# Performance work log

Hardware: AMD Instinct MI355X
Metric: run time of the kernel (lower is better)

The kernel has to match this reference:

```python
import jax, jax.numpy as jnp
import numpy as np

N = 4096   # num ROIs across the batch (sgdet: ~8 images x 512 proposals)
H = 256    # rl_input_size == rl_hidden_size (hard-coded in __init__)
C = 151    # Visual Genome object classes incl. background


def setup_inputs() -> dict:
    key = jax.random.key(0)
    ks = jax.random.split(key, 7)
    prepro_feat = jax.random.normal(ks[0], (N, H), jnp.float32)
    d = jax.random.uniform(ks[1], (N, C), jnp.float32)
    obj_distributions = d / d.sum(-1, keepdims=True)  # softmax-like class probs
    co_occour = jax.random.uniform(ks[2], (C, C), jnp.float32)
    W_sub = jax.random.normal(ks[3], (H, H), jnp.float32) / np.sqrt(H)
    b_sub = jnp.zeros((H,), jnp.float32)
    W_obj = jax.random.normal(ks[4], (H, H), jnp.float32) / np.sqrt(H)
    b_obj = jnp.zeros((H,), jnp.float32)
    w_scores = jax.random.normal(ks[5], (3 * H + 3,), jnp.float32) / np.sqrt(3 * H + 3)
    b_scores = jnp.zeros((), jnp.float32)
    return dict(prepro_feat=prepro_feat, obj_distributions=obj_distributions,
                co_occour=co_occour, W_sub=W_sub, b_sub=b_sub,
                W_obj=W_obj, b_obj=b_obj, w_scores=w_scores, b_scores=b_scores)


def reference(prepro_feat, obj_distributions, co_occour, W_sub, b_sub,
              W_obj, b_obj, w_scores, b_scores):
    n = prepro_feat.shape[0]
    h = W_sub.shape[1]
    # label_scores = co_occour.sum(1)
    label_scores = co_occour.sum(1)                                   # [C]
    # rl_sub/rl_obj Linear + ReLU. In the torch expand, pair (i,j) uses sub[j], obj[i].
    sub = jax.nn.relu(prepro_feat @ W_sub + b_sub)                    # [N,H]
    obj = jax.nn.relu(prepro_feat @ W_obj + b_obj)                    # [N,H]
    # pair_score[i,j] = sum_{a,b} dist[j,a] * dist[i,b] * co[a,b]  (detached)
    pair_score = jax.lax.stop_gradient(
        jnp.einsum('ja,ab,ib->ij', obj_distributions, co_occour, obj_distributions))  # [N,N]
    s = jax.lax.stop_gradient(obj_distributions @ label_scores)       # [N]
    sub_score = s[None, :]   # varies along j
    obj_score = s[:, None]   # varies along i
    # rl_scores Linear over concat(sub*obj, sub, obj, pair, sub_score, obj_score),
    # decomposed exactly into its blocks (avoids the [N,N,3H+3] intermediate).
    w_mul, w_s, w_o = w_scores[:h], w_scores[h:2 * h], w_scores[2 * h:3 * h]
    w_ps, w_ss, w_os = w_scores[3 * h], w_scores[3 * h + 1], w_scores[3 * h + 2]
    pair_out = ((obj * w_mul) @ sub.T                                 # [i,j] = sum_h obj[i,h]*sub[j,h]*w_mul[h]
                + (sub @ w_s)[None, :]
                + (obj @ w_o)[:, None]
                + w_ps * pair_score + w_ss * sub_score + w_os * obj_score
                + b_scores)                                           # [N,N]
    pair_gates = jax.nn.sigmoid(pair_out).reshape(-1, 1)              # [N*N, 1]
    return pair_gates
```

## Files before the change

kernel.cpp:

```cpp
#include <hip/hip_runtime.h>
#include <hip/hip_bf16.h>
#include <math.h>

#define N_DIM 4096
#define H_DIM 256
#define C_DIM 151
#define KP    448
#define KT    160

typedef unsigned short ushort_t;
typedef __attribute__((ext_vector_type(8))) short bf16x8;
typedef __attribute__((ext_vector_type(4))) float f32x4;

#define WSB_PPACK  0
#define WSB_WT     2097152
#define WSB_DPACK  2359296
#define WSB_COT    3670016
#define WSB_PART   3731456
#define WSB_SPART  3993600
#define WSB_APACK  4091904
#define WSB_BPACK  7761920

#define GLL(src, dst) __builtin_amdgcn_global_load_lds( \
    (const __attribute__((address_space(1))) void*)(src), \
    (__attribute__((address_space(3))) void*)(dst), 16, 0, 0)

__global__ __launch_bounds__(256) void k_cvt(
    const float* __restrict__ P, const float* __restrict__ Ws,
    const float* __restrict__ Wo, const float* __restrict__ D,
    const float* __restrict__ co, const float* __restrict__ wsc,
    __hip_bfloat16* __restrict__ Pp, __hip_bfloat16* __restrict__ Wt,
    __hip_bfloat16* __restrict__ Dpack, __hip_bfloat16* __restrict__ coT,
    __hip_bfloat16* __restrict__ Apack) {
    __shared__ float shbuf[64 * C_DIM];
    const int t = threadIdx.x;
    const int bid = blockIdx.x;
    if (bid < 512) {
        int idx = (bid * 256 + t) * 8;
        float4 a = *(const float4*)(P + idx);
        float4 b = *(const float4*)(P + idx + 4);
        __hip_bfloat16 h[8];
        h[0] = __float2bfloat16(a.x); h[1] = __float2bfloat16(a.y);
        h[2] = __float2bfloat16(a.z); h[3] = __float2bfloat16(a.w);
        h[4] = __float2bfloat16(b.x); h[5] = __float2bfloat16(b.y);
        h[6] = __float2bfloat16(b.z); h[7] = __float2bfloat16(b.w);
        *(bf16x8*)&Pp[idx] = *(bf16x8*)h;
    } else if (bid < 544) {
        const int b  = bid - 512;
        const int k0 = (b & 3) * 64;
        const int h0 = ((b >> 2) & 3) * 64;
        const int z  = b >> 4;
        const float* W = z ? Wo : Ws;
        #pragma unroll
        for (int q = 0; q < 4; ++q) {
            int r = (t >> 4) + q * 16;
            int c = (t & 15) * 4;
            float4 f = *(const float4*)&W[(size_t)(k0 + r) * H_DIM + h0 + c];
            shbuf[r * 65 + c] = f.x; shbuf[r * 65 + c + 1] = f.y;
            shbuf[r * 65 + c + 2] = f.z; shbuf[r * 65 + c + 3] = f.w;
        }
        __syncthreads();
        #pragma unroll
        for (int q = 0; q < 2; ++q) {
            int idx = t + q * 256;
            int h   = idx >> 3;
            int kc  = idx & 7;
            __hip_bfloat16 u[8];
            #pragma unroll
            for (int j = 0; j < 8; ++j)
                u[j] = __float2bfloat16(shbuf[(kc * 8 + j) * 65 + h]);
            *(bf16x8*)&Wt[((size_t)z * H_DIM + h0 + h) * H_DIM + k0 + kc * 8] = *(bf16x8*)u;
        }
    } else if (bid < 608) {
        const int b  = bid - 544;
        const int i0 = b * 64;
        for (int idx = t; idx < 64 * C_DIM; idx += 256)
            shbuf[idx] = D[(size_t)i0 * C_DIM + idx];
        __syncthreads();
        const float wps = wsc[768];
        for (int o = t; o < 64 * (KT / 8); o += 256) {
            int r = o / (KT / 8), ch = o % (KT / 8);
            __hip_bfloat16 u[8];
            #pragma unroll
            for (int j = 0; j < 8; ++j) {
                int k = ch * 8 + j;
                u[j] = __float2bfloat16(k < C_DIM ? shbuf[r * C_DIM + k] : 0.f);
            }
            *(bf16x8*)&Dpack[(size_t)(i0 + r) * KT + ch * 8] = *(bf16x8*)u;
        }
        for (int o = t; o < 64 * 24; o += 256) {
            int r = o / 24, ch = o % 24;
            __hip_bfloat16 u[8];
            #pragma unroll
            for (int j = 0; j < 8; ++j) {
                int c = ch * 8 + j;
                u[j] = __float2bfloat16(c < C_DIM ? wps * shbuf[r * C_DIM + c] : 0.f);
            }
            *(bf16x8*)&Apack[(size_t)(i0 + r) * KP + H_DIM + ch * 8] = *(bf16x8*)u;
        }
    } else {
        const int q  = bid - 608;
        const int a0 = (q % 3) * 64;
        const int c0 = (q / 3) * 64;
        for (int o = t; o < 64 * 64; o += 256) {
            int r = o >> 6, c = o & 63;
            float v = 0.f;
            if (a0 + r < C_DIM && c0 + c < C_DIM)
                v = co[(size_t)(a0 + r) * C_DIM + c0 + c];
            shbuf[r * 65 + c] = v;
        }
        __syncthreads();
        const int nch = (a0 == 128) ? 4 : 8;
        for (int o = t; o < 64 * 8; o += 256) {
            int cl = o >> 3, ch = o & 7;
            if (ch < nch) {
                __hip_bfloat16 u[8];
                #pragma unroll
                for (int j = 0; j < 8; ++j)
                    u[j] = __float2bfloat16(shbuf[(ch * 8 + j) * 65 + cl]);
                *(bf16x8*)&coT[(size_t)(c0 + cl) * KT + a0 + ch * 8] = *(bf16x8*)u;
            }
        }
    }
}

__global__ __launch_bounds__(256) void k_mid(
    const ushort_t* __restrict__ Pp, const ushort_t* __restrict__ Wt,
    const ushort_t* __restrict__ Dpack, const ushort_t* __restrict__ coT,
    const float* __restrict__ bsub, const float* __restrict__ bobj,
    const float* __restrict__ wsc,
    __hip_bfloat16* __restrict__ Apack, __hip_bfloat16* __restrict__ Bpack,
    float* __restrict__ part, float* __restrict__ spart) {
    __shared__ ushort_t As[128 * 256];
    __shared__ ushort_t Bs[64 * 256];

    const int t = threadIdx.x;
    const int w = t >> 6, l = t & 63;
    const int wr = w >> 1, wc = w & 1;
    const int lr = l & 15, g = l >> 4;
    const int bid = blockIdx.x;

    if (bid < 256) {
        const int hblk = bid & 3;
        const int i0   = ((bid >> 2) & 31) * 128;
        const int z    = bid >> 7;
        const int j0   = hblk * 64;
        const float* bias = z ? bobj : bsub;
        const ushort_t* Wz = Wt + (size_t)z * H_DIM * H_DIM;

        #pragma unroll
        for (int r_ = 0; r_ < 16; ++r_) {
            int idx = t + r_ * 256, row = idx >> 5, cl = idx & 31;
            int cs = cl ^ (row & 7);
            GLL(Pp + (size_t)(i0 + row) * H_DIM + cs * 8, &As[idx * 8]);
        }
        #pragma unroll
        for (int r_ = 0; r_ < 8; ++r_) {
            int idx = t + r_ * 256, row = idx >> 5, cl = idx & 31;
            int cs = cl ^ (row & 7);
            GLL(Wz + (size_t)(j0 + row) * H_DIM + cs * 8, &Bs[idx * 8]);
        }
        __syncthreads();

        f32x4 acc[4][2];
        #pragma unroll
        for (int m = 0; m < 4; ++m)
            #pragma unroll
            for (int n = 0; n < 2; ++n) acc[m][n] = f32x4{0.f, 0.f, 0.f, 0.f};

        #pragma unroll
        for (int ks2 = 0; ks2 < 8; ++ks2) {
            bf16x8 a[4], b[2];
            int c = ks2 * 4 + g;
            #pragma unroll
            for (int m = 0; m < 4; ++m) {
                int Rl = wr * 64 + m * 16 + lr;
                int cl = c ^ (Rl & 7);
                a[m] = *(const bf16x8*)&As[(Rl * 32 + cl) * 8];
            }
            #pragma unroll
            for (int n = 0; n < 2; ++n) {
                int Rl = wc * 32 + n * 16 + lr;
                int cl = c ^ (Rl & 7);
                b[n] = *(const bf16x8*)&Bs[(Rl * 32 + cl) * 8];
            }
            #pragma unroll
            for (int m = 0; m < 4; ++m)
                #pragma unroll
                for (int n = 0; n < 2; ++n)
                    acc[m][n] = __builtin_amdgcn_mfma_f32_16x16x32_bf16(
                        a[m], b[n], acc[m][n], 0, 0, 0);
        }

        int hn[2]; float bb[2], wse[2], wmu[2];
        #pragma unroll
        for (int n = 0; n < 2; ++n) {
            hn[n]  = j0 + wc * 32 + n * 16 + lr;
            bb[n]  = bias[hn[n]];
            wse[n] = wsc[(z ? 512 : 256) + hn[n]];
            wmu[n] = wsc[hn[n]];
        }
        float* partq = part + (size_t)(z * 8 + hblk * 2 + wc) * N_DIM;
        #pragma unroll
        for (int m = 0; m < 4; ++m) {
            float p[4] = {0.f, 0.f, 0.f, 0.f};
            #pragma unroll
            for (int n = 0; n < 2; ++n)
                #pragma unroll
                for (int r = 0; r < 4; ++r) {
                    float v = acc[m][n][r] + bb[n];
                    v = v > 0.f ? v : 0.f;
                    int i = i0 + wr * 64 + m * 16 + g * 4 + r;
                    if (z) Apack[(size_t)i * KP + hn[n]] = __float2bfloat16(v * wmu[n]);
                    else   Bpack[(size_t)i * KP + hn[n]] = __float2bfloat16(v);
                    p[r] += v * wse[n];
                }
            #pragma unroll
            for (int r = 0; r < 4; ++r) {
                p[r] += __shfl_xor(p[r], 1);
                p[r] += __shfl_xor(p[r], 2);
                p[r] += __shfl_xor(p[r], 4);
                p[r] += __shfl_xor(p[r], 8);
            }
            if (lr == 0)
                #pragma unroll
                for (int r = 0; r < 4; ++r)
                    partq[i0 + wr * 64 + m * 16 + g * 4 + r] = p[r];
        }
    } else {
        const int q  = bid - 256;
        const int j0 = (q % 3) * 64;
        const int i0 = (q / 3) * 64;

        bf16x8 a[2][5], b[2][5];
        #pragma unroll
        for (int m = 0; m < 2; ++m) {
            const ushort_t* ap = Dpack + (size_t)(i0 + wr * 32 + m * 16 + lr) * KT + g * 8;
            #pragma unroll
            for (int ks = 0; ks < 5; ++ks) a[m][ks] = *(const bf16x8*)(ap + ks * 32);
        }
        #pragma unroll
        for (int n = 0; n < 2; ++n) {
            const ushort_t* bp = coT + (size_t)(j0 + wc * 32 + n * 16 + lr) * KT + g * 8;
            #pragma unroll
            for (int ks = 0; ks < 5; ++ks) b[n][ks] = *(const bf16x8*)(bp + ks * 32);
        }

        f32x4 acc[2][2];
        #pragma unroll
        for (int m = 0; m < 2; ++m)
            #pragma unroll
            for (int n = 0; n < 2; ++n) acc[m][n] = f32x4{0.f, 0.f, 0.f, 0.f};
        #pragma unroll
        for (int ks = 0; ks < 5; ++ks)
            #pragma unroll
            for (int m = 0; m < 2; ++m)
                #pragma unroll
                for (int n = 0; n < 2; ++n)
                    acc[m][n] = __builtin_amdgcn_mfma_f32_16x16x32_bf16(
                        a[m][ks], b[n][ks], acc[m][n], 0, 0, 0);

        float* sp = spart + (size_t)((q % 3) * 2 + wc) * N_DIM;
        #pragma unroll
        for (int m = 0; m < 2; ++m) {
            float p[4] = {0.f, 0.f, 0.f, 0.f};
            #pragma unroll
            for (int n = 0; n < 2; ++n) {
                int col = j0 + wc * 32 + n * 16 + lr;
                #pragma unroll
                for (int r = 0; r < 4; ++r) {
                    int i = i0 + wr * 32 + m * 16 + g * 4 + r;
                    float v = acc[m][n][r];
                    Bpack[(size_t)i * KP + H_DIM + col] = __float2bfloat16(v);
                    p[r] += v;
                }
            }
            #pragma unroll
            for (int r = 0; r < 4; ++r) {
                p[r] += __shfl_xor(p[r], 1);
                p[r] += __shfl_xor(p[r], 2);
                p[r] += __shfl_xor(p[r], 4);
                p[r] += __shfl_xor(p[r], 8);
            }
            if (lr == 0)
                #pragma unroll
                for (int r = 0; r < 4; ++r)
                    sp[i0 + wr * 32 + m * 16 + g * 4 + r] = p[r];
        }
    }
}

__global__ __launch_bounds__(512) void k_main(
    const ushort_t* __restrict__ Apack, const ushort_t* __restrict__ Bpack,
    const float* __restrict__ part, const float* __restrict__ spart,
    const float* __restrict__ wsc, const float* __restrict__ bsc,
    float* __restrict__ out) {
    __shared__ ushort_t pool[(256 + 128) * 64];
    __shared__ float rbS[256], cbS[128];
    ushort_t* As = pool;
    ushort_t* Bs = pool + 256 * 64;

    const int t = threadIdx.x;
    const int w = t >> 6, l = t & 63;
    const int wm = w >> 1, wn = w & 1;
    const int lr = l & 15, g = l >> 4;
    const int bid = blockIdx.x;
    const int swz = (bid & 7) * 64 + (bid >> 3);
    const int i0 = (swz >> 5) * 256;
    const int j0 = (swz & 31) * 128;

#define K_STAGE(ks) do {                                                        \
    _Pragma("unroll")                                                           \
    for (int r_ = 0; r_ < 4; ++r_) {                                            \
        int idx_ = t + r_ * 512, row_ = idx_ >> 3, cl_ = idx_ & 7;              \
        int cs_ = cl_ ^ (row_ & 7);                                             \
        GLL(Apack + (size_t)(i0+row_)*KP + (ks)*64 + cs_*8, &As[idx_*8]);       \
    }                                                                           \
    _Pragma("unroll")                                                           \
    for (int r_ = 0; r_ < 2; ++r_) {                                            \
        int idx_ = t + r_ * 512, row_ = idx_ >> 3, cl_ = idx_ & 7;              \
        int cs_ = cl_ ^ (row_ & 7);                                             \
        GLL(Bpack + (size_t)(j0+row_)*KP + (ks)*64 + cs_*8, &Bs[idx_*8]);       \
    }                                                                           \
} while (0)

#define K_COMPUTE() do {                                                        \
    _Pragma("unroll")                                                           \
    for (int ks2 = 0; ks2 < 2; ++ks2) {                                         \
        bf16x8 a[4], b[4];                                                      \
        int c = ks2 * 4 + g;                                                    \
        _Pragma("unroll")                                                       \
        for (int m_ = 0; m_ < 4; ++m_) {                                        \
            int Rl = wm * 64 + m_ * 16 + lr;                                    \
            int cl = c ^ (Rl & 7);                                              \
            a[m_] = *(const bf16x8*)&As[(Rl * 8 + cl) * 8];                     \
        }                                                                       \
        _Pragma("unroll")                                                       \
        for (int n_ = 0; n_ < 4; ++n_) {                                        \
            int Rl = wn * 64 + n_ * 16 + lr;                                    \
            int cl = c ^ (Rl & 7);                                              \
            b[n_] = *(const bf16x8*)&Bs[(Rl * 8 + cl) * 8];                     \
        }                                                                       \
        _Pragma("unroll")                                                       \
        for (int m_ = 0; m_ < 4; ++m_)                                          \
            _Pragma("unroll")                                                   \
            for (int n_ = 0; n_ < 4; ++n_)                                      \
                acc[m_][n_] = __builtin_amdgcn_mfma_f32_16x16x32_bf16(          \
                    a[m_], b[n_], acc[m_][n_], 0, 0, 0);                        \
    }                                                                           \
} while (0)

    K_STAGE(0);
    if (t < 256) {
        int i = i0 + t; float r = 0.f, si = 0.f;
        #pragma unroll
        for (int q = 8; q < 16; ++q) r += part[(size_t)q * N_DIM + i];
        #pragma unroll
        for (int q = 0; q < 6; ++q) si += spart[(size_t)q * N_DIM + i];
        rbS[t] = r + wsc[770] * si;
    } else if (t < 384) {
        int j = j0 + (t - 256); float c = 0.f, sj = 0.f;
        #pragma unroll
        for (int q = 0; q < 8; ++q) c += part[(size_t)q * N_DIM + j];
        #pragma unroll
        for (int q = 0; q < 6; ++q) sj += spart[(size_t)q * N_DIM + j];
        cbS[t - 256] = c + wsc[769] * sj + bsc[0];
    }
    __syncthreads();

    f32x4 acc[4][4];
    #pragma unroll
    for (int m = 0; m < 4; ++m)
        #pragma unroll
        for (int n = 0; n < 4; ++n) acc[m][n] = f32x4{0.f, 0.f, 0.f, 0.f};

    #pragma unroll 1
    for (int ks = 0; ks < 7; ++ks) {
        K_COMPUTE();
        if (ks < 6) {
            __syncthreads();
            K_STAGE(ks + 1);
            __syncthreads();
        }
    }
    __syncthreads();
#undef K_STAGE
#undef K_COMPUTE

    float cbv[4];
    #pragma unroll
    for (int n = 0; n < 4; ++n) cbv[n] = cbS[wn * 64 + n * 16 + lr];
    float* OutS = (float*)pool;
    #pragma unroll
    for (int mc = 0; mc < 4; ++mc) {
        if (wm == mc) {
            #pragma unroll
            for (int m = 0; m < 4; ++m)
                #pragma unroll
                for (int n = 0; n < 4; ++n)
                    #pragma unroll
                    for (int r = 0; r < 4; ++r) {
                        int rl = m * 16 + g * 4 + r;
                        float v = acc[m][n][r] + rbS[mc * 64 + rl] + cbv[n];
                        float e = __expf(-v);
                        OutS[rl * 132 + wn * 64 + n * 16 + lr] =
                            __builtin_amdgcn_rcpf(1.0f + e);
                    }
        }
        __syncthreads();
        {
            int row = t >> 3, seg = t & 7;
            const float* rp = OutS + row * 132;
            float* op = out + (size_t)(i0 + mc * 64 + row) * N_DIM + j0;
            #pragma unroll
            for (int k = 0; k < 4; ++k) {
                float4 v4 = *(const float4*)(rp + (seg + 8 * k) * 4);
                *(float4*)(op + (seg + 8 * k) * 4) = v4;
            }
        }
        __syncthreads();
    }
}

extern "C" void kernel_launch(void* const* d_in, const int* in_sizes, int n_in,
                              void* d_out, int out_size, void* d_ws, size_t ws_size,
                              hipStream_t stream) {
    const float* prepro = (const float*)d_in[0];
    const float* D      = (const float*)d_in[1];
    const float* co     = (const float*)d_in[2];
    const float* Wsub   = (const float*)d_in[3];
    const float* bsub   = (const float*)d_in[4];
    const float* Wobj   = (const float*)d_in[5];
    const float* bobj   = (const float*)d_in[6];
    const float* wsc    = (const float*)d_in[7];
    const float* bsc    = (const float*)d_in[8];
    float* out = (float*)d_out;

    char* ws = (char*)d_ws;
    __hip_bfloat16* Ppack = (__hip_bfloat16*)(ws + WSB_PPACK);
    __hip_bfloat16* Wt    = (__hip_bfloat16*)(ws + WSB_WT);
    __hip_bfloat16* Dpack = (__hip_bfloat16*)(ws + WSB_DPACK);
    __hip_bfloat16* coT   = (__hip_bfloat16*)(ws + WSB_COT);
    float* part  = (float*)(ws + WSB_PART);
    float* spart = (float*)(ws + WSB_SPART);
    __hip_bfloat16* Apack = (__hip_bfloat16*)(ws + WSB_APACK);
    __hip_bfloat16* Bpack = (__hip_bfloat16*)(ws + WSB_BPACK);

    k_cvt<<<617, 256, 0, stream>>>(prepro, Wsub, Wobj, D, co, wsc,
                                   Ppack, Wt, Dpack, coT, Apack);
    k_mid<<<448, 256, 0, stream>>>(
        (const ushort_t*)Ppack, (const ushort_t*)Wt,
        (const ushort_t*)Dpack, (const ushort_t*)coT,
        bsub, bobj, wsc, Apack, Bpack, part, spart);
    k_main<<<512, 512, 0, stream>>>(
        (const ushort_t*)Apack, (const ushort_t*)Bpack, part, spart, wsc, bsc, out);
}
```

Baseline: 49.51 us.

## Double-buffer LDS K-tiles with async prefetch and interleave wave row mapping

Splits the main GEMM's LDS tile into two half-depth (32-wide K) buffers and prefetches the next K slice via global_load_lds while the current one is computed. The old version staged a full 64-wide slice between two block barriers each iteration. It also raises MFMA priority with s_setprio and remaps each wave's A rows (interleaved by 16 across four 64-row chunks), so every wave writes output in every epilogue chunk and no longer idles behind the `wm == mc` condition. The hand-written vmcnt/lgkmcnt waits and raw barriers replace __syncthreads, which is fragile if the compiler reorders memory ops. The initial rbS/cbS writes are now only ordered before their reads by the barriers inside the loop.

Measured after the change: 50.78 us (median of 3 runs). +2.6%, slower.

```diff
diff --git a/kernel.cpp b/kernel.cpp
--- a/kernel.cpp
+++ b/kernel.cpp
@@ -295,10 +295,8 @@
     const float* __restrict__ part, const float* __restrict__ spart,
     const float* __restrict__ wsc, const float* __restrict__ bsc,
     float* __restrict__ out) {
-    __shared__ ushort_t pool[(256 + 128) * 64];
+    __shared__ ushort_t pool[2][(256 + 128) * 32];
     __shared__ float rbS[256], cbS[128];
-    ushort_t* As = pool;
-    ushort_t* Bs = pool + 256 * 64;
 
     const int t = threadIdx.x;
     const int w = t >> 6, l = t & 63;
@@ -309,48 +307,6 @@
     const int i0 = (swz >> 5) * 256;
     const int j0 = (swz & 31) * 128;
 
-#define K_STAGE(ks) do {                                                        \
-    _Pragma("unroll")                                                           \
-    for (int r_ = 0; r_ < 4; ++r_) {                                            \
-        int idx_ = t + r_ * 512, row_ = idx_ >> 3, cl_ = idx_ & 7;              \
-        int cs_ = cl_ ^ (row_ & 7);                                             \
-        GLL(Apack + (size_t)(i0+row_)*KP + (ks)*64 + cs_*8, &As[idx_*8]);       \
-    }                                                                           \
-    _Pragma("unroll")                                                           \
-    for (int r_ = 0; r_ < 2; ++r_) {                                            \
-        int idx_ = t + r_ * 512, row_ = idx_ >> 3, cl_ = idx_ & 7;              \
-        int cs_ = cl_ ^ (row_ & 7);                                             \
-        GLL(Bpack + (size_t)(j0+row_)*KP + (ks)*64 + cs_*8, &Bs[idx_*8]);       \
-    }                                                                           \
-} while (0)
-
-#define K_COMPUTE() do {                                                        \
-    _Pragma("unroll")                                                           \
-    for (int ks2 = 0; ks2 < 2; ++ks2) {                                         \
-        bf16x8 a[4], b[4];                                                      \
-        int c = ks2 * 4 + g;                                                    \
-        _Pragma("unroll")                                                       \
-        for (int m_ = 0; m_ < 4; ++m_) {                                        \
-            int Rl = wm * 64 + m_ * 16 + lr;                                    \
-            int cl = c ^ (Rl & 7);                                              \
-            a[m_] = *(const bf16x8*)&As[(Rl * 8 + cl) * 8];                     \
-        }                                                                       \
-        _Pragma("unroll")                                                       \
-        for (int n_ = 0; n_ < 4; ++n_) {                                        \
-            int Rl = wn * 64 + n_ * 16 + lr;                                    \
-            int cl = c ^ (Rl & 7);                                              \
-            b[n_] = *(const bf16x8*)&Bs[(Rl * 8 + cl) * 8];                     \
-        }                                                                       \
-        _Pragma("unroll")                                                       \
-        for (int m_ = 0; m_ < 4; ++m_)                                          \
-            _Pragma("unroll")                                                   \
-            for (int n_ = 0; n_ < 4; ++n_)                                      \
-                acc[m_][n_] = __builtin_amdgcn_mfma_f32_16x16x32_bf16(          \
-                    a[m_], b[n_], acc[m_][n_], 0, 0, 0);                        \
-    }                                                                           \
-} while (0)
-
-    K_STAGE(0);
     if (t < 256) {
         int i = i0 + t; float r = 0.f, si = 0.f;
         #pragma unroll
@@ -366,7 +322,51 @@
         for (int q = 0; q < 6; ++q) sj += spart[(size_t)q * N_DIM + j];
         cbS[t - 256] = c + wsc[769] * sj + bsc[0];
     }
-    __syncthreads();
+    asm volatile("s_waitcnt lgkmcnt(0)" ::: "memory");
+
+#define K_STAGE(buf, ks) do {                                                   \
+    _Pragma("unroll")                                                           \
+    for (int r_ = 0; r_ < 2; ++r_) {                                            \
+        int idx_ = t + r_ * 512, row_ = idx_ >> 2, cl_ = idx_ & 3;              \
+        int cs_ = cl_ ^ (row_ & 3);                                             \
+        GLL(Apack + (size_t)(i0+row_)*KP + (ks)*32 + cs_*8,                     \
+            &pool[buf][idx_*8]);                                                \
+    }                                                                           \
+    {                                                                           \
+        int row_ = t >> 2, cl_ = t & 3;                                         \
+        int cs_ = cl_ ^ (row_ & 3);                                             \
+        GLL(Bpack + (size_t)(j0+row_)*KP + (ks)*32 + cs_*8,                     \
+            &pool[buf][256*32 + t*8]);                                          \
+    }                                                                           \
+} while (0)
+
+#define K_COMPUTE(cur) do {                                                     \
+    const ushort_t* As_ = pool[cur];                                            \
+    const ushort_t* Bs_ = pool[cur] + 256*32;                                   \
+    bf16x8 a[4], b[4];                                                          \
+    _Pragma("unroll")                                                           \
+    for (int m_ = 0; m_ < 4; ++m_) {                                            \
+        int Rl = m_ * 64 + wm * 16 + lr;               \
+        int cl = g ^ (Rl & 3);                                                  \
+        a[m_] = *(const bf16x8*)&As_[(Rl * 4 + cl) * 8];                        \
+    }                                                                           \
+    _Pragma("unroll")                                                           \
+    for (int n_ = 0; n_ < 4; ++n_) {                                            \
+        int Rl = wn * 64 + n_ * 16 + lr;                                        \
+        int cl = g ^ (Rl & 3);                                                  \
+        b[n_] = *(const bf16x8*)&Bs_[(Rl * 4 + cl) * 8];                        \
+    }                                                                           \
+    __builtin_amdgcn_s_setprio(1);                                              \
+    _Pragma("unroll")                                                           \
+    for (int m_ = 0; m_ < 4; ++m_)                                              \
+        _Pragma("unroll")                                                       \
+        for (int n_ = 0; n_ < 4; ++n_)                                          \
+            acc[m_][n_] = __builtin_amdgcn_mfma_f32_16x16x32_bf16(              \
+                a[m_], b[n_], acc[m_][n_], 0, 0, 0);                            \
+    __builtin_amdgcn_s_setprio(0);                                              \
+} while (0)
+
+    K_STAGE(0, 0);
 
     f32x4 acc[4][4];
     #pragma unroll
@@ -375,15 +375,18 @@
         for (int n = 0; n < 4; ++n) acc[m][n] = f32x4{0.f, 0.f, 0.f, 0.f};
 
     #pragma unroll 1
-    for (int ks = 0; ks < 7; ++ks) {
-        K_COMPUTE();
-        if (ks < 6) {
-            __syncthreads();
-            K_STAGE(ks + 1);
-            __syncthreads();
-        }
+    for (int ks = 0; ks < 14; ++ks) {
+        const int cur = ks & 1;
+        if (ks < 13) {
+            K_STAGE(cur ^ 1, ks + 1);
+            asm volatile("s_waitcnt vmcnt(3)" ::: "memory");
+        } else {
+            asm volatile("s_waitcnt vmcnt(0)" ::: "memory");
+        }
+        __builtin_amdgcn_s_barrier();
+        K_COMPUTE(cur);
+        __builtin_amdgcn_s_barrier();
     }
-    __syncthreads();
 #undef K_STAGE
 #undef K_COMPUTE
 
@@ -393,21 +396,19 @@
     float* OutS = (float*)pool;
     #pragma unroll
     for (int mc = 0; mc < 4; ++mc) {
-        if (wm == mc) {
-            #pragma unroll
-            for (int m = 0; m < 4; ++m)
-                #pragma unroll
-                for (int n = 0; n < 4; ++n)
-                    #pragma unroll
-                    for (int r = 0; r < 4; ++r) {
-                        int rl = m * 16 + g * 4 + r;
-                        float v = acc[m][n][r] + rbS[mc * 64 + rl] + cbv[n];
-                        float e = __expf(-v);
-                        OutS[rl * 132 + wn * 64 + n * 16 + lr] =
-                            __builtin_amdgcn_rcpf(1.0f + e);
-                    }
-        }
-        __syncthreads();
+        #pragma unroll
+        for (int n = 0; n < 4; ++n) {
+            #pragma unroll
+            for (int r = 0; r < 4; ++r) {
+                int rl = wm * 16 + g * 4 + r;
+                float v = acc[mc][n][r] + rbS[mc * 64 + rl] + cbv[n];
+                float e = __expf(-v);
+                OutS[rl * 132 + wn * 64 + n * 16 + lr] =
+                    __builtin_amdgcn_rcpf(1.0f + e);
+            }
+        }
+        asm volatile("s_waitcnt lgkmcnt(0)" ::: "memory");
+        __builtin_amdgcn_s_barrier();
         {
             int row = t >> 3, seg = t & 7;
             const float* rp = OutS + row * 132;
@@ -418,7 +419,8 @@
                 *(float4*)(op + (seg + 8 * k) * 4) = v4;
             }
         }
-        __syncthreads();
+        asm volatile("s_waitcnt lgkmcnt(0)" ::: "memory");
+        __builtin_amdgcn_s_barrier();
     }
 }
 
```

## Split GEMM epilogue into separate bf16 intermediate and elementwise sigmoid kernel

Applied to the files above, without the earlier changes.

The main GEMM kernel now writes its raw accumulator as bf16 tiles to a workspace instead of applying the bias and sigmoid and storing fp32 output through LDS. A new elementwise kernel reads those tiles, adds row and column biases (computed once per tile row and column into global buffers), applies the sigmoid and writes the fp32 output. This decouples the epilogue from the GEMM but adds a 32 MB intermediate round trip, an extra launch, and bf16 rounding of the logits. The new kernel's reads from the intermediate are strided and poorly coalesced.

New measurement: 120.2 us. +142.8%, slower.

```diff
diff --git a/kernel.cpp b/kernel.cpp
--- a/kernel.cpp
+++ b/kernel.cpp
@@ -11,6 +11,7 @@
 typedef unsigned short ushort_t;
 typedef __attribute__((ext_vector_type(8))) short bf16x8;
 typedef __attribute__((ext_vector_type(4))) float f32x4;
+typedef __attribute__((ext_vector_type(4))) ushort_t u16x4;
 
 #define WSB_PPACK  0
 #define WSB_WT     2097152
@@ -20,6 +21,9 @@
 #define WSB_SPART  3993600
 #define WSB_APACK  4091904
 #define WSB_BPACK  7761920
+#define WSB_RB     11468800
+#define WSB_CB     11485184
+#define WSB_Z      11501568
 
 #define GLL(src, dst) __builtin_amdgcn_global_load_lds( \
     (const __attribute__((address_space(1))) void*)(src), \
@@ -294,9 +298,9 @@
     const ushort_t* __restrict__ Apack, const ushort_t* __restrict__ Bpack,
     const float* __restrict__ part, const float* __restrict__ spart,
     const float* __restrict__ wsc, const float* __restrict__ bsc,
-    float* __restrict__ out) {
+    float* __restrict__ rb, float* __restrict__ cb,
+    ushort_t* __restrict__ Zt) {
     __shared__ ushort_t pool[(256 + 128) * 64];
-    __shared__ float rbS[256], cbS[128];
     ushort_t* As = pool;
     ushort_t* Bs = pool + 256 * 64;
 
@@ -351,20 +355,21 @@
 } while (0)
 
     K_STAGE(0);
-    if (t < 256) {
+    if ((swz & 31) == 0 && t < 256) {
         int i = i0 + t; float r = 0.f, si = 0.f;
         #pragma unroll
         for (int q = 8; q < 16; ++q) r += part[(size_t)q * N_DIM + i];
         #pragma unroll
         for (int q = 0; q < 6; ++q) si += spart[(size_t)q * N_DIM + i];
-        rbS[t] = r + wsc[770] * si;
-    } else if (t < 384) {
+        rb[i] = r + wsc[770] * si;
+    }
+    if ((swz >> 5) == 0 && t >= 256 && t < 384) {
         int j = j0 + (t - 256); float c = 0.f, sj = 0.f;
         #pragma unroll
         for (int q = 0; q < 8; ++q) c += part[(size_t)q * N_DIM + j];
         #pragma unroll
         for (int q = 0; q < 6; ++q) sj += spart[(size_t)q * N_DIM + j];
-        cbS[t - 256] = c + wsc[769] * sj + bsc[0];
+        cb[j] = c + wsc[769] * sj + bsc[0];
     }
     __syncthreads();
 
@@ -383,43 +388,47 @@
             __syncthreads();
         }
     }
-    __syncthreads();
 #undef K_STAGE
 #undef K_COMPUTE
 
-    float cbv[4];
+    ushort_t* Zw = Zt + (size_t)swz * 32768 + w * 4096;
     #pragma unroll
-    for (int n = 0; n < 4; ++n) cbv[n] = cbS[wn * 64 + n * 16 + lr];
-    float* OutS = (float*)pool;
+    for (int m = 0; m < 4; ++m) {
+        #pragma unroll
+        for (int n = 0; n < 4; ++n) {
+            __hip_bfloat16 h[4];
+            #pragma unroll
+            for (int r = 0; r < 4; ++r) h[r] = __float2bfloat16(acc[m][n][r]);
+            *(u16x4*)&Zw[(n * 16 + lr) * 64 + m * 16 + g * 4] = *(u16x4*)h;
+        }
+    }
+}
+
+__global__ __launch_bounds__(512) void k_out(
+    const ushort_t* __restrict__ Zt, const float* __restrict__ rb,
+    const float* __restrict__ cb, float* __restrict__ out) {
+    const int o = (blockIdx.x * 512 + threadIdx.x) * 8;
+    const int i = o >> 12, j = o & 4095;
+    const int swz = ((i >> 8) << 5) | (j >> 7);
+    const int w   = (((i >> 6) & 3) << 1) | ((j >> 6) & 1);
+    const int row64 = i & 63, c0 = j & 63;
+    const ushort_t* zb = Zt + (size_t)swz * 32768 + w * 4096 + row64;
+
+    const float rbi = rb[i];
+    float4 cb0 = *(const float4*)&cb[j];
+    float4 cb1 = *(const float4*)&cb[j + 4];
+
+    float res[8];
     #pragma unroll
-    for (int mc = 0; mc < 4; ++mc) {
-        if (wm == mc) {
-            #pragma unroll
-            for (int m = 0; m < 4; ++m)
-                #pragma unroll
-                for (int n = 0; n < 4; ++n)
-                    #pragma unroll
-                    for (int r = 0; r < 4; ++r) {
-                        int rl = m * 16 + g * 4 + r;
-                        float v = acc[m][n][r] + rbS[mc * 64 + rl] + cbv[n];
-                        float e = __expf(-v);
-                        OutS[rl * 132 + wn * 64 + n * 16 + lr] =
-                            __builtin_amdgcn_rcpf(1.0f + e);
-                    }
-        }
-        __syncthreads();
-        {
-            int row = t >> 3, seg = t & 7;
-            const float* rp = OutS + row * 132;
-            float* op = out + (size_t)(i0 + mc * 64 + row) * N_DIM + j0;
-            #pragma unroll
-            for (int k = 0; k < 4; ++k) {
-                float4 v4 = *(const float4*)(rp + (seg + 8 * k) * 4);
-                *(float4*)(op + (seg + 8 * k) * 4) = v4;
-            }
-        }
-        __syncthreads();
-    }
+    for (int u = 0; u < 8; ++u) {
+        float z = __uint_as_float((unsigned)zb[(size_t)(c0 + u) * 64] << 16);
+        float cbv = (u < 4) ? ((const float*)&cb0)[u] : ((const float*)&cb1)[u - 4];
+        float v = z + rbi + cbv;
+        float e = __expf(-v);
+        res[u] = __builtin_amdgcn_rcpf(1.0f + e);
+    }
+    *(float4*)&out[o]     = *(float4*)&res[0];
+    *(float4*)&out[o + 4] = *(float4*)&res[4];
 }
 
 extern "C" void kernel_launch(void* const* d_in, const int* in_sizes, int n_in,
@@ -445,6 +454,9 @@
     float* spart = (float*)(ws + WSB_SPART);
     __hip_bfloat16* Apack = (__hip_bfloat16*)(ws + WSB_APACK);
     __hip_bfloat16* Bpack = (__hip_bfloat16*)(ws + WSB_BPACK);
+    float* rb = (float*)(ws + WSB_RB);
+    float* cb = (float*)(ws + WSB_CB);
+    ushort_t* Zt = (ushort_t*)(ws + WSB_Z);
 
     k_cvt<<<617, 256, 0, stream>>>(prepro, Wsub, Wobj, D, co, wsc,
                                    Ppack, Wt, Dpack, coT, Apack);
@@ -453,5 +465,7 @@
         (const ushort_t*)Dpack, (const ushort_t*)coT,
         bsub, bobj, wsc, Apack, Bpack, part, spart);
     k_main<<<512, 512, 0, stream>>>(
-        (const ushort_t*)Apack, (const ushort_t*)Bpack, part, spart, wsc, bsc, out);
+        (const ushort_t*)Apack, (const ushort_t*)Bpack, part, spart, wsc, bsc,
+        rb, cb, Zt);
+    k_out<<<4096, 512, 0, stream>>>((const ushort_t*)Zt, rb, cb, out);
 }
```
